# Kernel optimization log

Measured on AMD Instinct MI355X. Metric: run time of the kernel, lower is better.

## Reference

```python
import jax, jax.numpy as jnp
import numpy as np

B, S, D = 2, 256, 256
EPS = 1e-6  # annotated-transformer LayerNorm: g*(x-mean)/(std+eps)+b, std unbiased


def setup_inputs() -> dict:
    key = jax.random.key(0)
    k0, k1 = jax.random.split(key, 2)
    context = jax.random.normal(k0, (B, S, D), jnp.float32)
    eos_mask = jnp.ones((B, S), jnp.int32)            # unused by forward (kept for signature fidelity)
    prior = jnp.array([0.3], jnp.float32)
    ln_g = jnp.ones((D,), jnp.float32)
    ln_b = jnp.zeros((D,), jnp.float32)
    fc_w = jax.random.normal(k1, (2 * D,), jnp.float32) * 0.02  # nn.Linear(2D, 1) weight (flattened)
    fc_b = jnp.zeros((1,), jnp.float32)
    return {"context": context, "eos_mask": eos_mask, "prior": prior,
            "ln_g": ln_g, "ln_b": ln_b, "fc_w": fc_w, "fc_b": fc_b}


def reference(context, eos_mask, prior, ln_g, ln_b, fc_w, fc_b):
    Bq, Sq, Dq = context.shape
    # LayerNorm (unbiased std, eps added to std)
    mu = context.mean(-1, keepdims=True)
    var = jnp.sum((context - mu) ** 2, axis=-1, keepdims=True) / (Dq - 1)
    x = ln_g * (context - mu) / (jnp.sqrt(var) + EPS) + ln_b          # [B,S,D]

    # context_mean[b,i,k,:] = mean of x[b, i..k] for k>=i, else 0.
    # (equivalent to the O(S^3) mean-mask bmm, computed via prefix sums)
    cs0 = jnp.concatenate([jnp.zeros((Bq, 1, Dq), x.dtype), jnp.cumsum(x, axis=1)], axis=1)  # [B,S+1,D]
    ar = jnp.arange(Sq)
    valid = ar[None, :] >= ar[:, None]                                # [S,S] triu (k>=i)
    cnt = jnp.where(valid, (ar[None, :] - ar[:, None] + 1), 1).astype(x.dtype)
    seg_sum = cs0[:, None, 1:, :] - cs0[:, :-1, None, :]              # [B,S,S,D] sum x[i..k]
    cm = jnp.where(valid[None, :, :, None], seg_sum / cnt[None, :, :, None], 0.0)

    # context1[b,i,k,:] = x[b,k,:], zeroed elementwise where cm == 0
    c1 = jnp.where(cm == 0.0, 0.0, x[:, None, :, :])                  # [B,S,S,D]

    w1, w2 = fc_w[:Dq], fc_w[Dq:]
    logits = (jnp.einsum('bikd,d->bik', c1, w1)
              + jnp.einsum('bikd,d->bik', cm, w2) + fc_b[0])          # [B,S,S]
    Mij = jax.nn.sigmoid(logits)
    Mij = prior[0] + (1.0 - prior[0]) * Mij

    # strictly-lower triangle -> 1, cumprod along k, keep triu
    Gfill = jnp.where(valid[None], Mij, 1.0)
    G = jnp.cumprod(Gfill, axis=2)
    G = jnp.where(valid[None], G, 0.0)
    G = G + jnp.swapaxes(G, 1, 2)
    diag = jnp.diagonal(G, axis1=1, axis2=2) - 1.0                    # [B,S]
    G = G - diag[:, :, None] * jnp.eye(Sq, dtype=G.dtype)[None]
    return (G, Mij)
```

## Files before the change

kernel.cpp:

```cpp
#include <hip/hip_runtime.h>
#include <math.h>

#define BB 2
#define SS 256
#define DD 256
#define EPSF 1e-6f

__device__ __forceinline__ float block_reduce_sum(float v, float* lds) {
    int t = threadIdx.x;
    lds[t] = v;
    __syncthreads();
    for (int s = 128; s > 0; s >>= 1) {
        if (t < s) lds[t] += lds[t + s];
        __syncthreads();
    }
    float r = lds[0];
    __syncthreads();
    return r;
}

__global__ void ln_dots_kernel(const float* __restrict__ ctx,
                               const float* __restrict__ ln_g,
                               const float* __restrict__ ln_b,
                               const float* __restrict__ fc_w,
                               float* __restrict__ dx1,
                               float* __restrict__ dx2) {
    __shared__ float lds[DD];
    const int r = blockIdx.x;
    const int t = threadIdx.x;
    const float c = ctx[r * DD + t];
    const float mu = block_reduce_sum(c, lds) * (1.0f / DD);
    const float dmu = c - mu;
    const float var = block_reduce_sum(dmu * dmu, lds) * (1.0f / (DD - 1));
    const float xn = ln_g[t] * dmu / (sqrtf(var) + EPSF) + ln_b[t];
    const float s1 = block_reduce_sum(xn * fc_w[t], lds);
    const float s2 = block_reduce_sum(xn * fc_w[DD + t], lds);
    if (t == 0) { dx1[r] = s1; dx2[r] = s2; }
}

__global__ void scan_kernel(const float* __restrict__ dx2, float* __restrict__ P2) {
    __shared__ float lds[SS];
    const int b = blockIdx.x, t = threadIdx.x;
    lds[t] = dx2[b * SS + t];
    __syncthreads();
    for (int o = 1; o < SS; o <<= 1) {
        float add = (t >= o) ? lds[t - o] : 0.0f;
        __syncthreads();
        lds[t] += add;
        __syncthreads();
    }
    P2[b * (SS + 1) + t + 1] = lds[t];
    if (t == 0) P2[b * (SS + 1)] = 0.0f;
}

__global__ void mij_g_kernel(const float* __restrict__ dx1,
                             const float* __restrict__ P2,
                             const float* __restrict__ prior,
                             const float* __restrict__ fc_b,
                             float* __restrict__ G,
                             float* __restrict__ Mij) {
    __shared__ float lds[SS];
    const int r = blockIdx.x;
    const int b = r / SS, i = r % SS;
    const int k = threadIdx.x;
    const float pr = prior[0], fb = fc_b[0];
    float m;
    if (k >= i) {
        const float base = P2[b * (SS + 1) + i];
        const float l = dx1[b * SS + k]
                      + (P2[b * (SS + 1) + k + 1] - base) / (float)(k - i + 1)
                      + fb;
        m = pr + (1.0f - pr) / (1.0f + expf(-l));
    } else {
        m = pr + (1.0f - pr) / (1.0f + expf(-fb));
    }
    Mij[r * SS + k] = m;

    lds[k] = (k >= i) ? m : 1.0f;
    __syncthreads();
    for (int o = 1; o < SS; o <<= 1) {
        float mul = (k >= o) ? lds[k - o] : 1.0f;
        __syncthreads();
        lds[k] *= mul;
        __syncthreads();
    }
    const float p = lds[k];

    if (k == i) {
        G[(b * SS + i) * SS + i] = 1.0f;
    } else if (k > i) {
        G[(b * SS + i) * SS + k] = p;
        G[(b * SS + k) * SS + i] = p;
    }
}

extern "C" void kernel_launch(void* const* d_in, const int* in_sizes, int n_in,
                              void* d_out, int out_size, void* d_ws, size_t ws_size,
                              hipStream_t stream) {
    const float* ctx   = (const float*)d_in[0];
    const float* prior = (const float*)d_in[2];
    const float* ln_g  = (const float*)d_in[3];
    const float* ln_b  = (const float*)d_in[4];
    const float* fc_w  = (const float*)d_in[5];
    const float* fc_b  = (const float*)d_in[6];

    float* G   = (float*)d_out;
    float* Mij = (float*)d_out + BB * SS * SS;

    float* dx1 = (float*)d_ws;
    float* dx2 = dx1 + BB * SS;
    float* P2  = dx2 + BB * SS;

    ln_dots_kernel<<<BB * SS, DD, 0, stream>>>(ctx, ln_g, ln_b, fc_w, dx1, dx2);
    scan_kernel<<<BB, SS, 0, stream>>>(dx2, P2);
    mij_g_kernel<<<BB * SS, SS, 0, stream>>>(dx1, P2, prior, fc_b, G, Mij);
}
```

Measured before the change: 15.59 us.

## Fuse three kernels into one cooperative kernel with wave-shuffle reductions and scans

Merges the LayerNorm/dot, prefix-scan and Mij/cumprod kernels into a single cooperative launch that uses a grid-wide sync between the per-row dot products and the rest. Every block recomputes the per-batch prefix sum of dx2 locally instead of running a separate scan kernel. LDS tree reductions and Hillis-Steele scans are replaced with 64-lane wave shuffles plus a small cross-wave combine. This removes two kernel launches and many __syncthreads barriers, at the cost of a grid barrier, redundant scan work in each block, and the requirement that all 512 blocks be co-resident.

```diff
diff --git a/kernel.cpp b/kernel.cpp
--- a/kernel.cpp
+++ b/kernel.cpp
@@ -1,90 +1,134 @@
 #include <hip/hip_runtime.h>
+#include <hip/hip_cooperative_groups.h>
 #include <math.h>
+
+namespace cg = cooperative_groups;
 
 #define BB 2
 #define SS 256
 #define DD 256
 #define EPSF 1e-6f
 
-__device__ __forceinline__ float block_reduce_sum(float v, float* lds) {
-    int t = threadIdx.x;
-    lds[t] = v;
+__device__ __forceinline__ float wave_sum(float v) {
+#pragma unroll
+    for (int o = 32; o > 0; o >>= 1) v += __shfl_xor(v, o);
+    return v;
+}
+
+__device__ __forceinline__ float block_sum(float v, float* lds) {
+    const int t = threadIdx.x, w = t >> 6, lane = t & 63;
+    v = wave_sum(v);
+    if (lane == 0) lds[w] = v;
     __syncthreads();
-    for (int s = 128; s > 0; s >>= 1) {
-        if (t < s) lds[t] += lds[t + s];
-        __syncthreads();
-    }
-    float r = lds[0];
+    float r = lds[0] + lds[1] + lds[2] + lds[3];
     __syncthreads();
     return r;
 }
 
-__global__ void ln_dots_kernel(const float* __restrict__ ctx,
-                               const float* __restrict__ ln_g,
-                               const float* __restrict__ ln_b,
-                               const float* __restrict__ fc_w,
-                               float* __restrict__ dx1,
-                               float* __restrict__ dx2) {
-    __shared__ float lds[DD];
-    const int r = blockIdx.x;
-    const int t = threadIdx.x;
-    const float c = ctx[r * DD + t];
-    const float mu = block_reduce_sum(c, lds) * (1.0f / DD);
-    const float dmu = c - mu;
-    const float var = block_reduce_sum(dmu * dmu, lds) * (1.0f / (DD - 1));
-    const float xn = ln_g[t] * dmu / (sqrtf(var) + EPSF) + ln_b[t];
-    const float s1 = block_reduce_sum(xn * fc_w[t], lds);
-    const float s2 = block_reduce_sum(xn * fc_w[DD + t], lds);
-    if (t == 0) { dx1[r] = s1; dx2[r] = s2; }
+__device__ __forceinline__ float2 block_sum2(float a, float b, float* lds) {
+    const int t = threadIdx.x, w = t >> 6, lane = t & 63;
+    a = wave_sum(a);
+    b = wave_sum(b);
+    if (lane == 0) { lds[w] = a; lds[4 + w] = b; }
+    __syncthreads();
+    float2 r;
+    r.x = lds[0] + lds[1] + lds[2] + lds[3];
+    r.y = lds[4] + lds[5] + lds[6] + lds[7];
+    __syncthreads();
+    return r;
 }
 
-__global__ void scan_kernel(const float* __restrict__ dx2, float* __restrict__ P2) {
-    __shared__ float lds[SS];
-    const int b = blockIdx.x, t = threadIdx.x;
-    lds[t] = dx2[b * SS + t];
-    __syncthreads();
-    for (int o = 1; o < SS; o <<= 1) {
-        float add = (t >= o) ? lds[t - o] : 0.0f;
-        __syncthreads();
-        lds[t] += add;
-        __syncthreads();
+__device__ __forceinline__ float wave_scan_sum(float v) {
+    const int lane = threadIdx.x & 63;
+#pragma unroll
+    for (int o = 1; o < 64; o <<= 1) {
+        float u = __shfl_up(v, o);
+        if (lane >= o) v += u;
     }
-    P2[b * (SS + 1) + t + 1] = lds[t];
-    if (t == 0) P2[b * (SS + 1)] = 0.0f;
+    return v;
 }
 
-__global__ void mij_g_kernel(const float* __restrict__ dx1,
-                             const float* __restrict__ P2,
+__device__ __forceinline__ float wave_scan_prod(float v) {
+    const int lane = threadIdx.x & 63;
+#pragma unroll
+    for (int o = 1; o < 64; o <<= 1) {
+        float u = __shfl_up(v, o);
+        if (lane >= o) v *= u;
+    }
+    return v;
+}
+
+__device__ __forceinline__ float block_scan_sum(float v, float* lds) {
+    const int t = threadIdx.x, w = t >> 6, lane = t & 63;
+    v = wave_scan_sum(v);
+    if (lane == 63) lds[w] = v;
+    __syncthreads();
+    float pre = 0.0f;
+#pragma unroll
+    for (int j = 0; j < 3; ++j)
+        if (w > j) pre += lds[j];
+    __syncthreads();
+    return v + pre;
+}
+
+__device__ __forceinline__ float block_scan_prod(float v, float* lds) {
+    const int t = threadIdx.x, w = t >> 6, lane = t & 63;
+    v = wave_scan_prod(v);
+    if (lane == 63) lds[w] = v;
+    __syncthreads();
+    float pre = 1.0f;
+#pragma unroll
+    for (int j = 0; j < 3; ++j)
+        if (w > j) pre *= lds[j];
+    __syncthreads();
+    return v * pre;
+}
+
+__global__ void fused_kernel(const float* __restrict__ ctx,
+                             const float* __restrict__ ln_g,
+                             const float* __restrict__ ln_b,
+                             const float* __restrict__ fc_w,
                              const float* __restrict__ prior,
                              const float* __restrict__ fc_b,
                              float* __restrict__ G,
-                             float* __restrict__ Mij) {
+                             float* __restrict__ Mij,
+                             float* __restrict__ dx1,
+                             float* __restrict__ dx2) {
     __shared__ float lds[SS];
     const int r = blockIdx.x;
-    const int b = r / SS, i = r % SS;
-    const int k = threadIdx.x;
+    const int t = threadIdx.x;
+
+    const float c  = ctx[r * DD + t];
+    const float mu = block_sum(c, lds) * (1.0f / DD);
+    const float dmu = c - mu;
+    const float var = block_sum(dmu * dmu, lds) * (1.0f / (DD - 1));
+    const float xn = ln_g[t] * dmu / (sqrtf(var) + EPSF) + ln_b[t];
+    const float2 s = block_sum2(xn * fc_w[t], xn * fc_w[DD + t], lds);
+    if (t == 0) { dx1[r] = s.x; dx2[r] = s.y; }
+
+    cg::this_grid().sync();
+
+    const int b = r >> 8, i = r & 255, k = t;
     const float pr = prior[0], fb = fc_b[0];
+
+    const float d2 = dx2[b * SS + k];
+    const float incl = block_scan_sum(d2, lds);
+    lds[k] = incl;
+    __syncthreads();
+    const float base = (i > 0) ? lds[i - 1] : 0.0f;
+    __syncthreads();
+
     float m;
     if (k >= i) {
-        const float base = P2[b * (SS + 1) + i];
-        const float l = dx1[b * SS + k]
-                      + (P2[b * (SS + 1) + k + 1] - base) / (float)(k - i + 1)
-                      + fb;
+        const float l = dx1[b * SS + k] + (incl - base) / (float)(k - i + 1) + fb;
         m = pr + (1.0f - pr) / (1.0f + expf(-l));
     } else {
         m = pr + (1.0f - pr) / (1.0f + expf(-fb));
     }
     Mij[r * SS + k] = m;
 
-    lds[k] = (k >= i) ? m : 1.0f;
-    __syncthreads();
-    for (int o = 1; o < SS; o <<= 1) {
-        float mul = (k >= o) ? lds[k - o] : 1.0f;
-        __syncthreads();
-        lds[k] *= mul;
-        __syncthreads();
-    }
-    const float p = lds[k];
+    const float v = (k >= i) ? m : 1.0f;
+    const float p = block_scan_prod(v, lds);
 
     if (k == i) {
         G[(b * SS + i) * SS + i] = 1.0f;
@@ -109,9 +153,10 @@
 
     float* dx1 = (float*)d_ws;
     float* dx2 = dx1 + BB * SS;
-    float* P2  = dx2 + BB * SS;
 
-    ln_dots_kernel<<<BB * SS, DD, 0, stream>>>(ctx, ln_g, ln_b, fc_w, dx1, dx2);
-    scan_kernel<<<BB, SS, 0, stream>>>(dx2, P2);
-    mij_g_kernel<<<BB * SS, SS, 0, stream>>>(dx1, P2, prior, fc_b, G, Mij);
+    void* args[] = {(void*)&ctx, (void*)&ln_g, (void*)&ln_b, (void*)&fc_w,
+                    (void*)&prior, (void*)&fc_b, (void*)&G, (void*)&Mij,
+                    (void*)&dx1, (void*)&dx2};
+    hipLaunchCooperativeKernel((void*)fused_kernel, dim3(BB * SS), dim3(SS),
+                               args, 0, stream);
 }
```

New measurement: 59.87 us. +284.1%, slower.

## Fuse prefix scan into Mij kernel and use wave-shuffle reductions and scans

Applied to the files above, without the earlier changes.

Removes the separate scan kernel: each Mij/G block now recomputes the prefix sum of dx2 itself using wave shuffle scans, which cuts one launch and the global round trip for P2. LayerNorm plus dot products are rewritten so each wave handles one row with float4 loads and shuffle reductions. The variance comes from a single-pass sum of squares, and the normalization is folded algebraically into the dot products. The cumulative product over k is also done as a wave scan instead of a barrier-heavy LDS loop. In exchange, every row block repeats the redundant prefix scan, and the single-pass variance may be less numerically stable.

```diff
diff --git a/kernel.cpp b/kernel.cpp
--- a/kernel.cpp
+++ b/kernel.cpp
@@ -6,91 +6,119 @@
 #define DD 256
 #define EPSF 1e-6f
 
-__device__ __forceinline__ float block_reduce_sum(float v, float* lds) {
-    int t = threadIdx.x;
-    lds[t] = v;
-    __syncthreads();
-    for (int s = 128; s > 0; s >>= 1) {
-        if (t < s) lds[t] += lds[t + s];
-        __syncthreads();
+__device__ __forceinline__ float wave_scan_sum(float v, int lane) {
+#pragma unroll
+    for (int o = 1; o < 64; o <<= 1) {
+        float u = __shfl_up(v, o);
+        if (lane >= o) v += u;
     }
-    float r = lds[0];
-    __syncthreads();
-    return r;
+    return v;
+}
+__device__ __forceinline__ float wave_scan_prod(float v, int lane) {
+#pragma unroll
+    for (int o = 1; o < 64; o <<= 1) {
+        float u = __shfl_up(v, o);
+        if (lane >= o) v *= u;
+    }
+    return v;
 }
 
-__global__ void ln_dots_kernel(const float* __restrict__ ctx,
-                               const float* __restrict__ ln_g,
-                               const float* __restrict__ ln_b,
-                               const float* __restrict__ fc_w,
-                               float* __restrict__ dx1,
-                               float* __restrict__ dx2) {
-    __shared__ float lds[DD];
-    const int r = blockIdx.x;
-    const int t = threadIdx.x;
-    const float c = ctx[r * DD + t];
-    const float mu = block_reduce_sum(c, lds) * (1.0f / DD);
-    const float dmu = c - mu;
-    const float var = block_reduce_sum(dmu * dmu, lds) * (1.0f / (DD - 1));
-    const float xn = ln_g[t] * dmu / (sqrtf(var) + EPSF) + ln_b[t];
-    const float s1 = block_reduce_sum(xn * fc_w[t], lds);
-    const float s2 = block_reduce_sum(xn * fc_w[DD + t], lds);
-    if (t == 0) { dx1[r] = s1; dx2[r] = s2; }
+__global__ __launch_bounds__(256) void k1_lndots(
+        const float* __restrict__ ctx,
+        const float* __restrict__ ln_g, const float* __restrict__ ln_b,
+        const float* __restrict__ fc_w,
+        float* __restrict__ dx1, float* __restrict__ dx2) {
+    const int t = threadIdx.x, wv = t >> 6, lane = t & 63;
+    const int r = blockIdx.x * 4 + wv;
+
+    const float4 c  = ((const float4*)ctx)[r * 64 + lane];
+    const float4 g  = ((const float4*)ln_g)[lane];
+    const float4 bb = ((const float4*)ln_b)[lane];
+    const float4 w1 = ((const float4*)fc_w)[lane];
+    const float4 w2 = ((const float4*)fc_w)[64 + lane];
+
+    const float gw1x = g.x * w1.x, gw1y = g.y * w1.y, gw1z = g.z * w1.z, gw1w = g.w * w1.w;
+    const float gw2x = g.x * w2.x, gw2y = g.y * w2.y, gw2z = g.z * w2.z, gw2w = g.w * w2.w;
+
+    float s0  = c.x + c.y + c.z + c.w;
+    float s1  = c.x * c.x + c.y * c.y + c.z * c.z + c.w * c.w;
+    float a1  = c.x * gw1x + c.y * gw1y + c.z * gw1z + c.w * gw1w;
+    float a2  = c.x * gw2x + c.y * gw2y + c.z * gw2z + c.w * gw2w;
+    float sg1 = gw1x + gw1y + gw1z + gw1w;
+    float sg2 = gw2x + gw2y + gw2z + gw2w;
+    float cb1 = bb.x * w1.x + bb.y * w1.y + bb.z * w1.z + bb.w * w1.w;
+    float cb2 = bb.x * w2.x + bb.y * w2.y + bb.z * w2.z + bb.w * w2.w;
+
+#pragma unroll
+    for (int o = 32; o > 0; o >>= 1) {
+        s0  += __shfl_xor(s0, o);
+        s1  += __shfl_xor(s1, o);
+        a1  += __shfl_xor(a1, o);
+        a2  += __shfl_xor(a2, o);
+        sg1 += __shfl_xor(sg1, o);
+        sg2 += __shfl_xor(sg2, o);
+        cb1 += __shfl_xor(cb1, o);
+        cb2 += __shfl_xor(cb2, o);
+    }
+
+    if (lane == 0) {
+        const float mu  = s0 * (1.0f / DD);
+        const float var = (s1 - DD * mu * mu) * (1.0f / (DD - 1));
+        const float inv = 1.0f / (sqrtf(var) + EPSF);
+        dx1[r] = (a1 - mu * sg1) * inv + cb1;
+        dx2[r] = (a2 - mu * sg2) * inv + cb2;
+    }
 }
 
-__global__ void scan_kernel(const float* __restrict__ dx2, float* __restrict__ P2) {
-    __shared__ float lds[SS];
-    const int b = blockIdx.x, t = threadIdx.x;
-    lds[t] = dx2[b * SS + t];
+__global__ __launch_bounds__(256) void k2_mg(
+        const float* __restrict__ dx1, const float* __restrict__ dx2,
+        const float* __restrict__ prior, const float* __restrict__ fc_b,
+        float* __restrict__ G, float* __restrict__ Mij) {
+    __shared__ float P2s[SS];
+    __shared__ float parts_s[4];
+    __shared__ float parts_p[4];
+
+    const int r = blockIdx.x;
+    const int b = r >> 8, i = r & 255;
+    const int t = threadIdx.x, wv = t >> 6, lane = t & 63;
+
+    const float d2 = dx2[b * SS + t];
+    const float d1 = dx1[b * SS + t];
+
+    float incl = wave_scan_sum(d2, lane);
+    if (lane == 63) parts_s[wv] = incl;
     __syncthreads();
-    for (int o = 1; o < SS; o <<= 1) {
-        float add = (t >= o) ? lds[t - o] : 0.0f;
-        __syncthreads();
-        lds[t] += add;
-        __syncthreads();
-    }
-    P2[b * (SS + 1) + t + 1] = lds[t];
-    if (t == 0) P2[b * (SS + 1)] = 0.0f;
-}
+#pragma unroll
+    for (int j = 0; j < 3; ++j)
+        if (wv > j) incl += parts_s[j];
+    P2s[t] = incl;
+    __syncthreads();
 
-__global__ void mij_g_kernel(const float* __restrict__ dx1,
-                             const float* __restrict__ P2,
-                             const float* __restrict__ prior,
-                             const float* __restrict__ fc_b,
-                             float* __restrict__ G,
-                             float* __restrict__ Mij) {
-    __shared__ float lds[SS];
-    const int r = blockIdx.x;
-    const int b = r / SS, i = r % SS;
-    const int k = threadIdx.x;
+    const float base = (i > 0) ? P2s[i - 1] : 0.0f;
     const float pr = prior[0], fb = fc_b[0];
+
     float m;
-    if (k >= i) {
-        const float base = P2[b * (SS + 1) + i];
-        const float l = dx1[b * SS + k]
-                      + (P2[b * (SS + 1) + k + 1] - base) / (float)(k - i + 1)
-                      + fb;
+    if (t >= i) {
+        const float l = d1 + (incl - base) / (float)(t - i + 1) + fb;
         m = pr + (1.0f - pr) / (1.0f + expf(-l));
     } else {
         m = pr + (1.0f - pr) / (1.0f + expf(-fb));
     }
-    Mij[r * SS + k] = m;
+    Mij[r * SS + t] = m;
 
-    lds[k] = (k >= i) ? m : 1.0f;
+    const float v = (t >= i) ? m : 1.0f;
+    float pincl = wave_scan_prod(v, lane);
+    if (lane == 63) parts_p[wv] = pincl;
     __syncthreads();
-    for (int o = 1; o < SS; o <<= 1) {
-        float mul = (k >= o) ? lds[k - o] : 1.0f;
-        __syncthreads();
-        lds[k] *= mul;
-        __syncthreads();
-    }
-    const float p = lds[k];
+#pragma unroll
+    for (int j = 0; j < 3; ++j)
+        if (wv > j) pincl *= parts_p[j];
 
-    if (k == i) {
-        G[(b * SS + i) * SS + i] = 1.0f;
-    } else if (k > i) {
-        G[(b * SS + i) * SS + k] = p;
-        G[(b * SS + k) * SS + i] = p;
+    if (t == i) {
+        G[r * SS + t] = 1.0f;
+    } else if (t > i) {
+        G[r * SS + t] = pincl;
+        G[(size_t)(b * SS + t) * SS + i] = pincl;
     }
 }
 
@@ -109,9 +137,7 @@
 
     float* dx1 = (float*)d_ws;
     float* dx2 = dx1 + BB * SS;
-    float* P2  = dx2 + BB * SS;
 
-    ln_dots_kernel<<<BB * SS, DD, 0, stream>>>(ctx, ln_g, ln_b, fc_w, dx1, dx2);
-    scan_kernel<<<BB, SS, 0, stream>>>(dx2, P2);
-    mij_g_kernel<<<BB * SS, SS, 0, stream>>>(dx1, P2, prior, fc_b, G, Mij);
+    k1_lndots<<<BB * SS / 4, 256, 0, stream>>>(ctx, ln_g, ln_b, fc_w, dx1, dx2);
+    k2_mg<<<BB * SS, 256, 0, stream>>>(dx1, dx2, prior, fc_b, G, Mij);
 }
```

Result: faster. 12.94 us (-17.0%).
